# Kernel tuning notes

Hardware: AMD Instinct MI355X
Metric: run time of the kernel (lower is better)

Reference implementation:

```python
import jax, jax.numpy as jnp
import numpy as np

B, N, E, D, R, T, L = 4, 20000, 320000, 64, 64, 1000, 6
LN_EPS = 1e-5


def setup_inputs() -> dict:
    key = jax.random.key(0)
    ks = jax.random.split(key, 20)
    inp = {
        "edge_index": jax.random.randint(ks[0], (2, E), 0, N),
        "edge_type": jax.random.randint(ks[1], (E,), 0, R),
        "relation_representations": jax.random.normal(ks[2], (B, R, D), jnp.float32),
        "h_index": jax.random.randint(ks[3], (B,), 0, N),
        "r_index": jax.random.randint(ks[4], (B,), 0, R),
        "t_index": jax.random.randint(ks[5], (B, T), 0, N),
        "edge_weight": jnp.ones((E,), jnp.float32),
        # per-layer relation-projection MLP (Linear,ReLU,Linear)
        "rp_w1": jax.random.normal(ks[6], (L, D, D), jnp.float32) / np.sqrt(D),
        "rp_b1": jnp.zeros((L, D), jnp.float32),
        "rp_w2": jax.random.normal(ks[7], (L, D, D), jnp.float32) / np.sqrt(D),
        "rp_b2": jnp.zeros((L, D), jnp.float32),
        # per-layer update linear: concat([input, aggregated]) -> D
        "conv_w": jax.random.normal(ks[8], (L, 2 * D, D), jnp.float32) / np.sqrt(2 * D),
        "conv_b": jnp.zeros((L, D), jnp.float32),
        "ln_g": jnp.ones((L, D), jnp.float32),
        "ln_b": jnp.zeros((L, D), jnp.float32),
        # final MLP (num_mlp_layers=2): feature_dim = D (last hidden) + D (query) = 2D
        "mlp_w1": jax.random.normal(ks[9], (2 * D, 2 * D), jnp.float32) / np.sqrt(2 * D),
        "mlp_b1": jnp.zeros((2 * D,), jnp.float32),
        "mlp_w2": jax.random.normal(ks[10], (2 * D, 1), jnp.float32) / np.sqrt(2 * D),
        "mlp_b2": jnp.zeros((1,), jnp.float32),
    }
    return inp


def reference(edge_index, edge_type, relation_representations, h_index, r_index,
              t_index, edge_weight, rp_w1, rp_b1, rp_w2, rp_b2, conv_w, conv_b,
              ln_g, ln_b, mlp_w1, mlp_b1, mlp_w2, mlp_b2):
    # --- boundary: scatter query embedding onto source node per query ---
    query = relation_representations[jnp.arange(B), r_index]              # [B, D]
    boundary = jnp.zeros((B, N, D), jnp.float32).at[jnp.arange(B), h_index].add(query)
    src, dst = edge_index[0], edge_index[1]

    def layer(x, params):
        w1, b1, w2, b2, cw, cb, g, b = params
        # project_relations MLP on query relation representations
        rel = jax.nn.relu(jnp.einsum('brd,de->bre', relation_representations, w1) + b1)
        rel = jnp.einsum('brd,de->bre', rel, w2) + b2                     # [B, R, D]
        # distmult message: h[src] * rel[edge_type], weighted
        msg = x[:, src, :] * rel[:, edge_type, :] * edge_weight[None, :, None]  # [B, E, D]
        agg = jax.ops.segment_sum(msg.transpose(1, 0, 2), dst,
                                  num_segments=N).transpose(1, 0, 2)
        agg = agg + boundary                                              # boundary self-loop
        h = jnp.concatenate([x, agg], axis=-1) @ cw + cb                  # [B, N, D]
        mu = h.mean(-1, keepdims=True)
        var = h.var(-1, keepdims=True)
        h = (h - mu) * jax.lax.rsqrt(var + LN_EPS) * g + b                # layer norm
        h = jax.nn.relu(h)
        return h + x, None                                                # short_cut

    x, _ = jax.lax.scan(layer, boundary,
                        (rp_w1, rp_b1, rp_w2, rp_b2, conv_w, conv_b, ln_g, ln_b))
    node_query = jnp.broadcast_to(query[:, None, :], (B, N, D))
    output = jnp.concatenate([x, node_query], axis=-1)                    # [B, N, 2D]
    feat = jnp.take_along_axis(output, t_index[:, :, None], axis=1)       # [B, T, 2D]
    h = jax.nn.relu(feat @ mlp_w1 + mlp_b1)
    score = (h @ mlp_w2 + mlp_b2).squeeze(-1)                             # [B, T]
    return score
```

## Files before the change

### kernel.cpp

```cpp
#include <hip/hip_runtime.h>
#include <hip/hip_fp16.h>

#define NB 4
#define NN 20000
#define NE 320000
#define ND 64
#define NR 64
#define NT 1000
#define NL 6
#define LN_EPS 1e-5f
#define CAP 64

typedef _Float16 half8 __attribute__((ext_vector_type(8)));
typedef _Float16 half4v __attribute__((ext_vector_type(4)));
typedef float floatx4 __attribute__((ext_vector_type(4)));


__global__ void __launch_bounds__(256)
prep1(int* __restrict__ cnt,
      const float* __restrict__ cw, _Float16* __restrict__ cwt,
      const float* __restrict__ relrep, const int* __restrict__ r_index,
      float* __restrict__ query,
      const float* __restrict__ rp_w1, const float* __restrict__ rp_b1,
      const float* __restrict__ rp_w2, const float* __restrict__ rp_b2,
      __half* __restrict__ rel16) {
    int blk = blockIdx.x, tid = threadIdx.x;
    if (blk < 79) {
        int i = blk * 256 + tid;
        if (i < NN) cnt[i] = 0;
    } else if (blk < 271) {
        int i = (blk - 79) * 256 + tid;
        int l = i >> 13, rem = i & 8191, k = rem >> 6, n = rem & 63;
        cwt[l * 8192 + n * 128 + k] = (_Float16)cw[i];
    } else if (blk == 271) {
        int b = tid >> 6, d = tid & 63;
        query[tid] = relrep[(b * NR + r_index[b]) * ND + d];
    } else {
        int u = blk - 272;
        int l = u >> 6, r = u & 63;
        int b = tid >> 6, j = tid & 63;
        const float* w1 = rp_w1 + l * ND * ND;
        const float* w2 = rp_w2 + l * ND * ND;
        float xin = relrep[(b * NR + r) * ND + j];
        float acc = rp_b1[l * ND + j];
        #pragma unroll 8
        for (int k = 0; k < ND; ++k) acc += __shfl(xin, k) * w1[k * ND + j];
        float hmid = fmaxf(acc, 0.f);
        float outv = rp_b2[l * ND + j];
        #pragma unroll 8
        for (int k = 0; k < ND; ++k) outv += __shfl(hmid, k) * w2[k * ND + j];
        rel16[l * (NR * NB * ND) + (r * NB + b) * ND + j] = __float2half(outv);
    }
}

__global__ void __launch_bounds__(256)
prep2(const int* __restrict__ ei, const int* __restrict__ et,
      const float* __restrict__ ew, int* __restrict__ cnt,
      int4* __restrict__ epack) {
    int e = blockIdx.x * 256 + threadIdx.x;
    int d = ei[NE + e];
    int p = atomicAdd(&cnt[d], 1);
    if (p < CAP)
        epack[d * CAP + p] = make_int4(ei[e], et[e], __float_as_int(ew[e]), 0);
}

__device__ __forceinline__ float2 h2f(unsigned u) {
    __half2 h = *(__half2*)&u;
    return __half22float2(h);
}
__device__ __forceinline__ __half2 u2h2(unsigned u) { return *(__half2*)&u; }

__device__ __forceinline__ void conv_ln_epilogue(
        _Float16* A16, float* sD, int wv, int lane, int n,
        const _Float16* __restrict__ cwt, const float* __restrict__ cb,
        const float* __restrict__ g, const float* __restrict__ bb,
        __half* __restrict__ xo16) {
    __syncthreads();
    {
        int m = lane & 15, quad = lane >> 4;
        int ncol = wv * 16 + m;
        floatx4 acc = {0.f, 0.f, 0.f, 0.f};
        #pragma unroll
        for (int k0 = 0; k0 < 128; k0 += 32) {
            half8 a = *(const half8*)&A16[m * 136 + k0 + quad * 8];
            half8 bfr = *(const half8*)&cwt[ncol * 128 + k0 + quad * 8];
            acc = __builtin_amdgcn_mfma_f32_16x16x32_f16(a, bfr, acc, 0, 0, 0);
        }
        #pragma unroll
        for (int rg = 0; rg < 4; ++rg)
            sD[(quad * 4 + rg) * 65 + ncol] = acc[rg];
    }
    __syncthreads();
    float gl = g[lane], bl = bb[lane], cbl = cb[lane];
    #pragma unroll
    for (int b = 0; b < NB; ++b) {
        float acc = sD[(wv * 4 + b) * 65 + lane] + cbl;
        float s = acc, s2 = acc * acc;
        #pragma unroll
        for (int o = 32; o > 0; o >>= 1) { s += __shfl_xor(s, o); s2 += __shfl_xor(s2, o); }
        float mu  = s * (1.f / ND);
        float var = s2 * (1.f / ND) - mu * mu;
        float hn  = (acc - mu) * rsqrtf(var + LN_EPS) * gl + bl;
        float xvf = (float)A16[(wv * 4 + b) * 136 + lane];
        float v   = fmaxf(hn, 0.f) + xvf;
        xo16[(n * NB + b) * ND + lane] = __float2half(v);
    }
}

__global__ void __launch_bounds__(256)
fused_layer_first(const __half* __restrict__ rel16,
                  const int* __restrict__ cnt, const int4* __restrict__ epack,
                  const float* __restrict__ query, const int* __restrict__ h_index,
                  const _Float16* __restrict__ cwt, const float* __restrict__ cb,
                  const float* __restrict__ g, const float* __restrict__ bb,
                  __half* __restrict__ xo16) {
    __shared__ _Float16 A16[16 * 136];
    __shared__ float sD[16 * 65];
    int wv = threadIdx.x >> 6;
    int lane = threadIdx.x & 63;
    int n = blockIdx.x * 4 + wv;
    int cn = __builtin_amdgcn_readfirstlane(min(cnt[n], CAP));
    int bidx = lane >> 4, c4 = (lane & 15) << 2;
    int hb = h_index[bidx];

    const uint2* __restrict__ r2 = (const uint2*)rel16;
    float4 q4 = ((const float4*)query)[lane];
    half4v qh;
    qh.x = (_Float16)q4.x; qh.y = (_Float16)q4.y;
    qh.z = (_Float16)q4.z; qh.w = (_Float16)q4.w;
    float qx = (float)qh.x, qy = (float)qh.y, qz = (float)qh.z, qw = (float)qh.w;

    float4 agg4 = make_float4(0.f, 0.f, 0.f, 0.f);
    {
        int4 ed = make_int4(0, 0, 0, 0);
        if (lane < cn) ed = epack[n * CAP + lane];
        for (int j = 0; j < cn; ++j) {
            int s   = __builtin_amdgcn_readlane(ed.x, j);
            int t   = __builtin_amdgcn_readlane(ed.y, j);
            float w = __int_as_float(__builtin_amdgcn_readlane(ed.z, j));
            if (s == hb) {
                uint2 ra = r2[t * 64 + lane];
                float2 q0 = h2f(ra.x), q1 = h2f(ra.y);
                agg4.x = fmaf(qx * q0.x, w, agg4.x);
                agg4.y = fmaf(qy * q0.y, w, agg4.y);
                agg4.z = fmaf(qz * q1.x, w, agg4.z);
                agg4.w = fmaf(qw * q1.y, w, agg4.w);
            }
        }
    }
    if (n == hb) {
        agg4.x += q4.x; agg4.y += q4.y; agg4.z += q4.z; agg4.w += q4.w;
    }
    {
        int r = wv * 4 + bidx;
        half4v xh = {0, 0, 0, 0};
        if (n == hb) xh = qh;
        *(half4v*)&A16[r * 136 + c4] = xh;
        half4v ah;
        ah.x = (_Float16)agg4.x; ah.y = (_Float16)agg4.y;
        ah.z = (_Float16)agg4.z; ah.w = (_Float16)agg4.w;
        *(half4v*)&A16[r * 136 + 64 + c4] = ah;
    }
    conv_ln_epilogue(A16, sD, wv, lane, n, cwt, cb, g, bb, xo16);
}

__global__ void __launch_bounds__(256)
fused_layer(const __half* __restrict__ x16, const __half* __restrict__ rel16,
            const int* __restrict__ cnt, const int4* __restrict__ epack,
            const float* __restrict__ query, const int* __restrict__ h_index,
            const _Float16* __restrict__ cwt, const float* __restrict__ cb,
            const float* __restrict__ g, const float* __restrict__ bb,
            __half* __restrict__ xo16) {
    __shared__ _Float16 A16[16 * 136];
    __shared__ float sD[16 * 65];
    int wv = threadIdx.x >> 6;
    int lane = threadIdx.x & 63;
    int n = blockIdx.x * 4 + wv;
    int cn = __builtin_amdgcn_readfirstlane(min(cnt[n], CAP));
    int bidx = lane >> 4, c4 = (lane & 15) << 2;
    int hb = h_index[bidx];

    const uint2* __restrict__ x2 = (const uint2*)x16;
    const uint2* __restrict__ r2 = (const uint2*)rel16;

    uint2 xraw = x2[n * 64 + lane];

    float4 acc = make_float4(0.f, 0.f, 0.f, 0.f);
    {
        int4 ed = make_int4(0, 0, 0, 0);
        if (lane < cn) ed = epack[n * CAP + lane];
        for (int j = 0; j < cn; ++j) {
            int s   = __builtin_amdgcn_readlane(ed.x, j);
            int t   = __builtin_amdgcn_readlane(ed.y, j);
            float w = __int_as_float(__builtin_amdgcn_readlane(ed.z, j));
            uint2 xa = x2[s * 64 + lane];
            uint2 ra = r2[t * 64 + lane];
            __half2 p0 = __hmul2(u2h2(xa.x), u2h2(ra.x));
            __half2 p1 = __hmul2(u2h2(xa.y), u2h2(ra.y));
            acc.x = fmaf(__low2float(p0),  w, acc.x);
            acc.y = fmaf(__high2float(p0), w, acc.y);
            acc.z = fmaf(__low2float(p1),  w, acc.z);
            acc.w = fmaf(__high2float(p1), w, acc.w);
        }
    }
    if (n == hb) {
        const float4 q4 = ((const float4*)query)[lane];
        acc.x += q4.x; acc.y += q4.y; acc.z += q4.z; acc.w += q4.w;
    }
    {
        int r = wv * 4 + bidx;
        half4v ah;
        ah.x = (_Float16)acc.x; ah.y = (_Float16)acc.y;
        ah.z = (_Float16)acc.z; ah.w = (_Float16)acc.w;
        *(half4v*)&A16[r * 136 + 64 + c4] = ah;
        *(uint2*)&A16[r * 136 + c4] = xraw;
    }
    conv_ln_epilogue(A16, sD, wv, lane, n, cwt, cb, g, bb, xo16);
}

__global__ void final_score(const __half* __restrict__ x16, const float* __restrict__ query,
                            const int* __restrict__ t_index,
                            const float* __restrict__ w1, const float* __restrict__ b1,
                            const float* __restrict__ w2, const float* __restrict__ b2,
                            float* __restrict__ out) {
    int gid = blockIdx.x * 4 + (threadIdx.x >> 6);
    int lane = threadIdx.x & 63;
    int b = gid / NT;
    int ti = t_index[gid];
    float xv = __half2float(x16[(ti * NB + b) * ND + lane]);
    float qv = query[b * ND + lane];
    float a0 = b1[lane], a1 = b1[lane + 64];
    #pragma unroll 8
    for (int k = 0; k < ND; ++k) {
        float f = __shfl(xv, k);
        a0 += f * w1[k * 128 + lane];
        a1 += f * w1[k * 128 + lane + 64];
    }
    #pragma unroll 8
    for (int k = 0; k < ND; ++k) {
        float f = __shfl(qv, k);
        a0 += f * w1[(ND + k) * 128 + lane];
        a1 += f * w1[(ND + k) * 128 + lane + 64];
    }
    a0 = fmaxf(a0, 0.f);
    a1 = fmaxf(a1, 0.f);
    float p = a0 * w2[lane] + a1 * w2[lane + 64];
    #pragma unroll
    for (int o = 32; o > 0; o >>= 1) p += __shfl_xor(p, o);
    if (lane == 0) out[gid] = p + b2[0];
}

extern "C" void kernel_launch(void* const* d_in, const int* in_sizes, int n_in,
                              void* d_out, int out_size, void* d_ws, size_t ws_size,
                              hipStream_t stream) {
    const int*   edge_index  = (const int*)d_in[0];
    const int*   edge_type   = (const int*)d_in[1];
    const float* relrep      = (const float*)d_in[2];
    const int*   h_index     = (const int*)d_in[3];
    const int*   r_index     = (const int*)d_in[4];
    const int*   t_index     = (const int*)d_in[5];
    const float* edge_weight = (const float*)d_in[6];
    const float* rp_w1  = (const float*)d_in[7];
    const float* rp_b1  = (const float*)d_in[8];
    const float* rp_w2  = (const float*)d_in[9];
    const float* rp_b2  = (const float*)d_in[10];
    const float* conv_w = (const float*)d_in[11];
    const float* conv_b = (const float*)d_in[12];
    const float* ln_g   = (const float*)d_in[13];
    const float* ln_b   = (const float*)d_in[14];
    const float* mlp_w1 = (const float*)d_in[15];
    const float* mlp_b1 = (const float*)d_in[16];
    const float* mlp_w2 = (const float*)d_in[17];
    const float* mlp_b2 = (const float*)d_in[18];
    float* out = (float*)d_out;

    const int BND = NB * NN * ND;
    const int RELSZ = NR * NB * ND;
    float*    ws     = (float*)d_ws;
    float*    query  = ws;
    __half*   rel16  = (__half*)(query + 256);
    __half*   x16a   = rel16 + NL * RELSZ;
    __half*   x16b   = x16a + BND;
    _Float16* cwt16  = (_Float16*)(x16b + BND);
    int4*     epack  = (int4*)(cwt16 + NL * 8192);
    int*      cnt    = (int*)(epack + NN * CAP);

    prep1<<<656, 256, 0, stream>>>(cnt, conv_w, cwt16, relrep, r_index, query,
                                   rp_w1, rp_b1, rp_w2, rp_b2, rel16);
    prep2<<<NE / 256, 256, 0, stream>>>(edge_index, edge_type, edge_weight,
                                        cnt, epack);

    __half* mc = x16a; __half* mn = x16b;
    fused_layer_first<<<NN / 4, 256, 0, stream>>>(rel16, cnt, epack,
                                                  query, h_index,
                                                  cwt16, conv_b, ln_g, ln_b, mc);
    for (int l = 1; l < NL; ++l) {
        fused_layer<<<NN / 4, 256, 0, stream>>>(mc, rel16 + l * RELSZ, cnt, epack,
                                                query, h_index,
                                                cwt16 + l * 8192, conv_b + l * ND,
                                                ln_g + l * ND, ln_b + l * ND, mn);
        __half* th = mc; mc = mn; mn = th;
    }
    final_score<<<NB * NT / 4, 256, 0, stream>>>(mc, query, t_index,
                                                 mlp_w1, mlp_b1, mlp_w2, mlp_b2, out);
}
```

Before: 358.2 us.

## Stage per-layer relation table in LDS and double block size to eight nodes

Each block now cooperatively copies the layer's 32 KB fp16 relation table (R*B*D) into shared memory and serves per-edge relation gathers from LDS instead of global memory. Blocks grow from 4 to 8 waves (two groups of 4 nodes) to spread the staging cost over more nodes. This costs a 32 KB LDS copy per block and an extra barrier, which may cap occupancy and add traffic, though the table likely already sat in L2.

```diff
diff --git a/kernel.cpp b/kernel.cpp
--- a/kernel.cpp
+++ b/kernel.cpp
@@ -71,59 +71,71 @@
 __device__ __forceinline__ __half2 u2h2(unsigned u) { return *(__half2*)&u; }
 
 __device__ __forceinline__ void conv_ln_epilogue(
-        _Float16* A16, float* sD, int wv, int lane, int n,
+        _Float16* A16g, float* sDg, int wvl, int lane, int n,
         const _Float16* __restrict__ cwt, const float* __restrict__ cb,
         const float* __restrict__ g, const float* __restrict__ bb,
         __half* __restrict__ xo16) {
     __syncthreads();
     {
         int m = lane & 15, quad = lane >> 4;
-        int ncol = wv * 16 + m;
+        int ncol = wvl * 16 + m;
         floatx4 acc = {0.f, 0.f, 0.f, 0.f};
         #pragma unroll
         for (int k0 = 0; k0 < 128; k0 += 32) {
-            half8 a = *(const half8*)&A16[m * 136 + k0 + quad * 8];
+            half8 a = *(const half8*)&A16g[m * 136 + k0 + quad * 8];
             half8 bfr = *(const half8*)&cwt[ncol * 128 + k0 + quad * 8];
             acc = __builtin_amdgcn_mfma_f32_16x16x32_f16(a, bfr, acc, 0, 0, 0);
         }
         #pragma unroll
         for (int rg = 0; rg < 4; ++rg)
-            sD[(quad * 4 + rg) * 65 + ncol] = acc[rg];
+            sDg[(quad * 4 + rg) * 65 + ncol] = acc[rg];
     }
     __syncthreads();
     float gl = g[lane], bl = bb[lane], cbl = cb[lane];
     #pragma unroll
     for (int b = 0; b < NB; ++b) {
-        float acc = sD[(wv * 4 + b) * 65 + lane] + cbl;
+        float acc = sDg[(wvl * 4 + b) * 65 + lane] + cbl;
         float s = acc, s2 = acc * acc;
         #pragma unroll
         for (int o = 32; o > 0; o >>= 1) { s += __shfl_xor(s, o); s2 += __shfl_xor(s2, o); }
         float mu  = s * (1.f / ND);
         float var = s2 * (1.f / ND) - mu * mu;
         float hn  = (acc - mu) * rsqrtf(var + LN_EPS) * gl + bl;
-        float xvf = (float)A16[(wv * 4 + b) * 136 + lane];
+        float xvf = (float)A16g[(wvl * 4 + b) * 136 + lane];
         float v   = fmaxf(hn, 0.f) + xvf;
         xo16[(n * NB + b) * ND + lane] = __float2half(v);
     }
 }
 
-__global__ void __launch_bounds__(256)
+__global__ void __launch_bounds__(512)
 fused_layer_first(const __half* __restrict__ rel16,
                   const int* __restrict__ cnt, const int4* __restrict__ epack,
                   const float* __restrict__ query, const int* __restrict__ h_index,
                   const _Float16* __restrict__ cwt, const float* __restrict__ cb,
                   const float* __restrict__ g, const float* __restrict__ bb,
                   __half* __restrict__ xo16) {
-    __shared__ _Float16 A16[16 * 136];
-    __shared__ float sD[16 * 65];
-    int wv = threadIdx.x >> 6;
-    int lane = threadIdx.x & 63;
-    int n = blockIdx.x * 4 + wv;
+    __shared__ _Float16 relS[NR * NB * ND];
+    __shared__ _Float16 A16[2][16 * 136];
+    __shared__ float sD[2][16 * 65];
+    int tid = threadIdx.x;
+    int wv = tid >> 6, lane = tid & 63;
+    int grp = wv >> 2, wvl = wv & 3;
+    int n = blockIdx.x * 8 + wv;
     int cn = __builtin_amdgcn_readfirstlane(min(cnt[n], CAP));
     int bidx = lane >> 4, c4 = (lane & 15) << 2;
     int hb = h_index[bidx];
 
-    const uint2* __restrict__ r2 = (const uint2*)rel16;
+    int4 ed = make_int4(0, 0, 0, 0);
+    if (lane < cn) ed = epack[n * CAP + lane];
+
+    {
+        const uint4* rg4 = (const uint4*)rel16;
+        uint4* rs4 = (uint4*)relS;
+        #pragma unroll
+        for (int k = 0; k < 4; ++k) rs4[tid + 512 * k] = rg4[tid + 512 * k];
+    }
+    __syncthreads();
+
     float4 q4 = ((const float4*)query)[lane];
     half4v qh;
     qh.x = (_Float16)q4.x; qh.y = (_Float16)q4.y;
@@ -131,91 +143,96 @@
     float qx = (float)qh.x, qy = (float)qh.y, qz = (float)qh.z, qw = (float)qh.w;
 
     float4 agg4 = make_float4(0.f, 0.f, 0.f, 0.f);
-    {
-        int4 ed = make_int4(0, 0, 0, 0);
-        if (lane < cn) ed = epack[n * CAP + lane];
-        for (int j = 0; j < cn; ++j) {
-            int s   = __builtin_amdgcn_readlane(ed.x, j);
-            int t   = __builtin_amdgcn_readlane(ed.y, j);
-            float w = __int_as_float(__builtin_amdgcn_readlane(ed.z, j));
-            if (s == hb) {
-                uint2 ra = r2[t * 64 + lane];
-                float2 q0 = h2f(ra.x), q1 = h2f(ra.y);
-                agg4.x = fmaf(qx * q0.x, w, agg4.x);
-                agg4.y = fmaf(qy * q0.y, w, agg4.y);
-                agg4.z = fmaf(qz * q1.x, w, agg4.z);
-                agg4.w = fmaf(qw * q1.y, w, agg4.w);
-            }
+    const uint2* __restrict__ rS2 = (const uint2*)relS;
+    for (int j = 0; j < cn; ++j) {
+        int s   = __builtin_amdgcn_readlane(ed.x, j);
+        int t   = __builtin_amdgcn_readlane(ed.y, j);
+        float w = __int_as_float(__builtin_amdgcn_readlane(ed.z, j));
+        if (s == hb) {
+            uint2 ra = rS2[t * 64 + lane];
+            float2 q0 = h2f(ra.x), q1 = h2f(ra.y);
+            agg4.x = fmaf(qx * q0.x, w, agg4.x);
+            agg4.y = fmaf(qy * q0.y, w, agg4.y);
+            agg4.z = fmaf(qz * q1.x, w, agg4.z);
+            agg4.w = fmaf(qw * q1.y, w, agg4.w);
         }
     }
     if (n == hb) {
         agg4.x += q4.x; agg4.y += q4.y; agg4.z += q4.z; agg4.w += q4.w;
     }
     {
-        int r = wv * 4 + bidx;
+        int r = wvl * 4 + bidx;
         half4v xh = {0, 0, 0, 0};
         if (n == hb) xh = qh;
-        *(half4v*)&A16[r * 136 + c4] = xh;
+        *(half4v*)&A16[grp][r * 136 + c4] = xh;
         half4v ah;
         ah.x = (_Float16)agg4.x; ah.y = (_Float16)agg4.y;
         ah.z = (_Float16)agg4.z; ah.w = (_Float16)agg4.w;
-        *(half4v*)&A16[r * 136 + 64 + c4] = ah;
-    }
-    conv_ln_epilogue(A16, sD, wv, lane, n, cwt, cb, g, bb, xo16);
-}
-
-__global__ void __launch_bounds__(256)
+        *(half4v*)&A16[grp][r * 136 + 64 + c4] = ah;
+    }
+    conv_ln_epilogue(A16[grp], sD[grp], wvl, lane, n, cwt, cb, g, bb, xo16);
+}
+
+__global__ void __launch_bounds__(512)
 fused_layer(const __half* __restrict__ x16, const __half* __restrict__ rel16,
             const int* __restrict__ cnt, const int4* __restrict__ epack,
             const float* __restrict__ query, const int* __restrict__ h_index,
             const _Float16* __restrict__ cwt, const float* __restrict__ cb,
             const float* __restrict__ g, const float* __restrict__ bb,
             __half* __restrict__ xo16) {
-    __shared__ _Float16 A16[16 * 136];
-    __shared__ float sD[16 * 65];
-    int wv = threadIdx.x >> 6;
-    int lane = threadIdx.x & 63;
-    int n = blockIdx.x * 4 + wv;
+    __shared__ _Float16 relS[NR * NB * ND];
+    __shared__ _Float16 A16[2][16 * 136];
+    __shared__ float sD[2][16 * 65];
+    int tid = threadIdx.x;
+    int wv = tid >> 6, lane = tid & 63;
+    int grp = wv >> 2, wvl = wv & 3;
+    int n = blockIdx.x * 8 + wv;
     int cn = __builtin_amdgcn_readfirstlane(min(cnt[n], CAP));
     int bidx = lane >> 4, c4 = (lane & 15) << 2;
     int hb = h_index[bidx];
 
     const uint2* __restrict__ x2 = (const uint2*)x16;
-    const uint2* __restrict__ r2 = (const uint2*)rel16;
-
+
+    int4 ed = make_int4(0, 0, 0, 0);
+    if (lane < cn) ed = epack[n * CAP + lane];
     uint2 xraw = x2[n * 64 + lane];
 
+    {
+        const uint4* rg4 = (const uint4*)rel16;
+        uint4* rs4 = (uint4*)relS;
+        #pragma unroll
+        for (int k = 0; k < 4; ++k) rs4[tid + 512 * k] = rg4[tid + 512 * k];
+    }
+    __syncthreads();
+
     float4 acc = make_float4(0.f, 0.f, 0.f, 0.f);
-    {
-        int4 ed = make_int4(0, 0, 0, 0);
-        if (lane < cn) ed = epack[n * CAP + lane];
-        for (int j = 0; j < cn; ++j) {
-            int s   = __builtin_amdgcn_readlane(ed.x, j);
-            int t   = __builtin_amdgcn_readlane(ed.y, j);
-            float w = __int_as_float(__builtin_amdgcn_readlane(ed.z, j));
-            uint2 xa = x2[s * 64 + lane];
-            uint2 ra = r2[t * 64 + lane];
-            __half2 p0 = __hmul2(u2h2(xa.x), u2h2(ra.x));
-            __half2 p1 = __hmul2(u2h2(xa.y), u2h2(ra.y));
-            acc.x = fmaf(__low2float(p0),  w, acc.x);
-            acc.y = fmaf(__high2float(p0), w, acc.y);
-            acc.z = fmaf(__low2float(p1),  w, acc.z);
-            acc.w = fmaf(__high2float(p1), w, acc.w);
-        }
+    const uint2* __restrict__ rS2 = (const uint2*)relS;
+    for (int j = 0; j < cn; ++j) {
+        int s   = __builtin_amdgcn_readlane(ed.x, j);
+        int t   = __builtin_amdgcn_readlane(ed.y, j);
+        float w = __int_as_float(__builtin_amdgcn_readlane(ed.z, j));
+        uint2 xa = x2[s * 64 + lane];
+        uint2 ra = rS2[t * 64 + lane];
+        __half2 p0 = __hmul2(u2h2(xa.x), u2h2(ra.x));
+        __half2 p1 = __hmul2(u2h2(xa.y), u2h2(ra.y));
+        acc.x = fmaf(__low2float(p0),  w, acc.x);
+        acc.y = fmaf(__high2float(p0), w, acc.y);
+        acc.z = fmaf(__low2float(p1),  w, acc.z);
+        acc.w = fmaf(__high2float(p1), w, acc.w);
     }
     if (n == hb) {
         const float4 q4 = ((const float4*)query)[lane];
         acc.x += q4.x; acc.y += q4.y; acc.z += q4.z; acc.w += q4.w;
     }
     {
-        int r = wv * 4 + bidx;
+        int r = wvl * 4 + bidx;
         half4v ah;
         ah.x = (_Float16)acc.x; ah.y = (_Float16)acc.y;
         ah.z = (_Float16)acc.z; ah.w = (_Float16)acc.w;
-        *(half4v*)&A16[r * 136 + 64 + c4] = ah;
-        *(uint2*)&A16[r * 136 + c4] = xraw;
-    }
-    conv_ln_epilogue(A16, sD, wv, lane, n, cwt, cb, g, bb, xo16);
+        *(half4v*)&A16[grp][r * 136 + 64 + c4] = ah;
+        *(uint2*)&A16[grp][r * 136 + c4] = xraw;
+    }
+    conv_ln_epilogue(A16[grp], sD[grp], wvl, lane, n, cwt, cb, g, bb, xo16);
 }
 
 __global__ void final_score(const __half* __restrict__ x16, const float* __restrict__ query,
@@ -291,11 +308,11 @@
                                         cnt, epack);
 
     __half* mc = x16a; __half* mn = x16b;
-    fused_layer_first<<<NN / 4, 256, 0, stream>>>(rel16, cnt, epack,
+    fused_layer_first<<<NN / 8, 512, 0, stream>>>(rel16, cnt, epack,
                                                   query, h_index,
                                                   cwt16, conv_b, ln_g, ln_b, mc);
     for (int l = 1; l < NL; ++l) {
-        fused_layer<<<NN / 4, 256, 0, stream>>>(mc, rel16 + l * RELSZ, cnt, epack,
+        fused_layer<<<NN / 8, 512, 0, stream>>>(mc, rel16 + l * RELSZ, cnt, epack,
                                                 query, h_index,
                                                 cwt16 + l * 8192, conv_b + l * ND,
                                                 ln_g + l * ND, ln_b + l * ND, mn);
```

After: 429.1 us. 19.8% more time.

## Split edge gather across half-waves per batch and use 512-thread blocks

Applied to the files above, without the earlier changes.

The non-first layer kernel now loops over the four batches separately. In each step the two half-waves gather two different edges, using 4-byte loads of one batch slice, and their partial sums are combined with a cross-half shuffle. Blocks grow to 8 nodes (512 threads), with per-group shared-memory tiles for the MFMA/LayerNorm epilogue. The aim is more independent gathers in flight per wave. The cost is twice as many loop iterations and narrower, less vectorised loads, with padding reads when an odd edge count pairs with an empty lane.

```diff
diff --git a/kernel.cpp b/kernel.cpp
--- a/kernel.cpp
+++ b/kernel.cpp
@@ -71,37 +71,37 @@
 __device__ __forceinline__ __half2 u2h2(unsigned u) { return *(__half2*)&u; }
 
 __device__ __forceinline__ void conv_ln_epilogue(
-        _Float16* A16, float* sD, int wv, int lane, int n,
+        _Float16* A16g, float* sDg, int wvl, int lane, int n,
         const _Float16* __restrict__ cwt, const float* __restrict__ cb,
         const float* __restrict__ g, const float* __restrict__ bb,
         __half* __restrict__ xo16) {
     __syncthreads();
     {
         int m = lane & 15, quad = lane >> 4;
-        int ncol = wv * 16 + m;
+        int ncol = wvl * 16 + m;
         floatx4 acc = {0.f, 0.f, 0.f, 0.f};
         #pragma unroll
         for (int k0 = 0; k0 < 128; k0 += 32) {
-            half8 a = *(const half8*)&A16[m * 136 + k0 + quad * 8];
+            half8 a = *(const half8*)&A16g[m * 136 + k0 + quad * 8];
             half8 bfr = *(const half8*)&cwt[ncol * 128 + k0 + quad * 8];
             acc = __builtin_amdgcn_mfma_f32_16x16x32_f16(a, bfr, acc, 0, 0, 0);
         }
         #pragma unroll
         for (int rg = 0; rg < 4; ++rg)
-            sD[(quad * 4 + rg) * 65 + ncol] = acc[rg];
+            sDg[(quad * 4 + rg) * 65 + ncol] = acc[rg];
     }
     __syncthreads();
     float gl = g[lane], bl = bb[lane], cbl = cb[lane];
     #pragma unroll
     for (int b = 0; b < NB; ++b) {
-        float acc = sD[(wv * 4 + b) * 65 + lane] + cbl;
+        float acc = sDg[(wvl * 4 + b) * 65 + lane] + cbl;
         float s = acc, s2 = acc * acc;
         #pragma unroll
         for (int o = 32; o > 0; o >>= 1) { s += __shfl_xor(s, o); s2 += __shfl_xor(s2, o); }
         float mu  = s * (1.f / ND);
         float var = s2 * (1.f / ND) - mu * mu;
         float hn  = (acc - mu) * rsqrtf(var + LN_EPS) * gl + bl;
-        float xvf = (float)A16[(wv * 4 + b) * 136 + lane];
+        float xvf = (float)A16g[(wvl * 4 + b) * 136 + lane];
         float v   = fmaxf(hn, 0.f) + xvf;
         xo16[(n * NB + b) * ND + lane] = __float2half(v);
     }
@@ -164,58 +164,62 @@
     conv_ln_epilogue(A16, sD, wv, lane, n, cwt, cb, g, bb, xo16);
 }
 
-__global__ void __launch_bounds__(256)
+__global__ void __launch_bounds__(512)
 fused_layer(const __half* __restrict__ x16, const __half* __restrict__ rel16,
             const int* __restrict__ cnt, const int4* __restrict__ epack,
             const float* __restrict__ query, const int* __restrict__ h_index,
             const _Float16* __restrict__ cwt, const float* __restrict__ cb,
             const float* __restrict__ g, const float* __restrict__ bb,
             __half* __restrict__ xo16) {
-    __shared__ _Float16 A16[16 * 136];
-    __shared__ float sD[16 * 65];
-    int wv = threadIdx.x >> 6;
-    int lane = threadIdx.x & 63;
-    int n = blockIdx.x * 4 + wv;
+    __shared__ _Float16 A16[2][16 * 136];
+    __shared__ float sD[2][16 * 65];
+    int tid = threadIdx.x;
+    int wv = tid >> 6, lane = tid & 63;
+    int grp = wv >> 2, wvl = wv & 3;
+    int n = blockIdx.x * 8 + wv;
     int cn = __builtin_amdgcn_readfirstlane(min(cnt[n], CAP));
-    int bidx = lane >> 4, c4 = (lane & 15) << 2;
-    int hb = h_index[bidx];
-
-    const uint2* __restrict__ x2 = (const uint2*)x16;
-    const uint2* __restrict__ r2 = (const uint2*)rel16;
-
-    uint2 xraw = x2[n * 64 + lane];
-
-    float4 acc = make_float4(0.f, 0.f, 0.f, 0.f);
-    {
-        int4 ed = make_int4(0, 0, 0, 0);
-        if (lane < cn) ed = epack[n * CAP + lane];
-        for (int j = 0; j < cn; ++j) {
-            int s   = __builtin_amdgcn_readlane(ed.x, j);
-            int t   = __builtin_amdgcn_readlane(ed.y, j);
-            float w = __int_as_float(__builtin_amdgcn_readlane(ed.z, j));
-            uint2 xa = x2[s * 64 + lane];
-            uint2 ra = r2[t * 64 + lane];
-            __half2 p0 = __hmul2(u2h2(xa.x), u2h2(ra.x));
-            __half2 p1 = __hmul2(u2h2(xa.y), u2h2(ra.y));
-            acc.x = fmaf(__low2float(p0),  w, acc.x);
-            acc.y = fmaf(__high2float(p0), w, acc.y);
-            acc.z = fmaf(__low2float(p1),  w, acc.z);
-            acc.w = fmaf(__high2float(p1), w, acc.w);
-        }
-    }
-    if (n == hb) {
-        const float4 q4 = ((const float4*)query)[lane];
-        acc.x += q4.x; acc.y += q4.y; acc.z += q4.z; acc.w += q4.w;
-    }
-    {
-        int r = wv * 4 + bidx;
-        half4v ah;
-        ah.x = (_Float16)acc.x; ah.y = (_Float16)acc.y;
-        ah.z = (_Float16)acc.z; ah.w = (_Float16)acc.w;
-        *(half4v*)&A16[r * 136 + 64 + c4] = ah;
-        *(uint2*)&A16[r * 136 + c4] = xraw;
-    }
-    conv_ln_epilogue(A16, sD, wv, lane, n, cwt, cb, g, bb, xo16);
+    int hf = lane >> 5, sub = lane & 31;
+
+    const uint* __restrict__ xu = (const uint*)x16;
+    const uint* __restrict__ ru = (const uint*)rel16;
+
+    int4 ed = make_int4(0, 0, 0, 0);
+    if (lane < cn) ed = epack[n * CAP + lane];
+
+    for (int b = 0; b < NB; ++b) {
+        float ax = 0.f, ay = 0.f;
+        for (int j = 0; j < cn; j += 2) {
+            int s0 = __builtin_amdgcn_readlane(ed.x, j);
+            int s1 = __builtin_amdgcn_readlane(ed.x, j + 1);
+            int t0 = __builtin_amdgcn_readlane(ed.y, j);
+            int t1 = __builtin_amdgcn_readlane(ed.y, j + 1);
+            int w0 = __builtin_amdgcn_readlane(ed.z, j);
+            int w1 = __builtin_amdgcn_readlane(ed.z, j + 1);
+            int s = hf ? s1 : s0;
+            int t = hf ? t1 : t0;
+            float w = __int_as_float(hf ? w1 : w0);
+            uint xa = xu[(s * NB + b) * 32 + sub];
+            uint ra = ru[(t * NB + b) * 32 + sub];
+            __half2 p = __hmul2(u2h2(xa), u2h2(ra));
+            ax = fmaf(__low2float(p),  w, ax);
+            ay = fmaf(__high2float(p), w, ay);
+        }
+        ax += __shfl_xor(ax, 32);
+        ay += __shfl_xor(ay, 32);
+        if (n == h_index[b]) {
+            float2 q = ((const float2*)query)[b * 32 + sub];
+            ax += q.x; ay += q.y;
+        }
+        int r = wvl * 4 + b;
+        if (hf == 0) {
+            __half2 ah;
+            ah.x = __float2half(ax); ah.y = __float2half(ay);
+            *(__half2*)&A16[grp][r * 136 + 64 + 2 * sub] = ah;
+            uint xr = xu[(n * NB + b) * 32 + sub];
+            *(uint*)&A16[grp][r * 136 + 2 * sub] = xr;
+        }
+    }
+    conv_ln_epilogue(A16[grp], sD[grp], wvl, lane, n, cwt, cb, g, bb, xo16);
 }
 
 __global__ void final_score(const __half* __restrict__ x16, const float* __restrict__ query,
@@ -295,7 +299,7 @@
                                                   query, h_index,
                                                   cwt16, conv_b, ln_g, ln_b, mc);
     for (int l = 1; l < NL; ++l) {
-        fused_layer<<<NN / 4, 256, 0, stream>>>(mc, rel16 + l * RELSZ, cnt, epack,
+        fused_layer<<<NN / 8, 512, 0, stream>>>(mc, rel16 + l * RELSZ, cnt, epack,
                                                 query, h_index,
                                                 cwt16 + l * 8192, conv_b + l * ND,
                                                 ln_g + l * ND, ln_b + l * ND, mn);
```

New measurement: 520.6 us. 45.3% more time.

## Switch node features to batch-major layout and split fused layer per batch

Applied to the files above, without the earlier changes.

Changes the x and relation buffers from node-major [N,B,D] to batch-major [B,N,D] and packs source and edge type into one int, shrinking edge records from int4 to int2. The fused layer now runs one batch per block over 16 nodes, with half-waves gathering 128-byte rows per edge, and pairs adjacent blocks of the same batch. The aim is to cut edge-metadata traffic and improve L2 locality, since each block now touches only one batch's 2.5MB feature slab. The cost is that edge lists are re-read once per batch, and only half the waves do the MFMA step.

```diff
diff --git a/kernel.cpp b/kernel.cpp
--- a/kernel.cpp
+++ b/kernel.cpp
@@ -49,19 +49,20 @@
         float outv = rp_b2[l * ND + j];
         #pragma unroll 8
         for (int k = 0; k < ND; ++k) outv += __shfl(hmid, k) * w2[k * ND + j];
-        rel16[l * (NR * NB * ND) + (r * NB + b) * ND + j] = __float2half(outv);
+        rel16[l * (NR * NB * ND) + (b * NR + r) * ND + j] = __float2half(outv);
     }
 }
 
 __global__ void __launch_bounds__(256)
 prep2(const int* __restrict__ ei, const int* __restrict__ et,
       const float* __restrict__ ew, int* __restrict__ cnt,
-      int4* __restrict__ epack) {
+      int2* __restrict__ ep2) {
     int e = blockIdx.x * 256 + threadIdx.x;
     int d = ei[NE + e];
     int p = atomicAdd(&cnt[d], 1);
     if (p < CAP)
-        epack[d * CAP + p] = make_int4(ei[e], et[e], __float_as_int(ew[e]), 0);
+        ep2[d * CAP + p] = make_int2(ei[e] | (et[e] << 16),
+                                     __float_as_int(ew[e]));
 }
 
 __device__ __forceinline__ float2 h2f(unsigned u) {
@@ -70,7 +71,7 @@
 }
 __device__ __forceinline__ __half2 u2h2(unsigned u) { return *(__half2*)&u; }
 
-__device__ __forceinline__ void conv_ln_epilogue(
+__device__ __forceinline__ void conv_ln_epilogue4(
         _Float16* A16, float* sD, int wv, int lane, int n,
         const _Float16* __restrict__ cwt, const float* __restrict__ cb,
         const float* __restrict__ g, const float* __restrict__ bb,
@@ -103,13 +104,13 @@
         float hn  = (acc - mu) * rsqrtf(var + LN_EPS) * gl + bl;
         float xvf = (float)A16[(wv * 4 + b) * 136 + lane];
         float v   = fmaxf(hn, 0.f) + xvf;
-        xo16[(n * NB + b) * ND + lane] = __float2half(v);
+        xo16[(b * NN + n) * ND + lane] = __float2half(v);
     }
 }
 
 __global__ void __launch_bounds__(256)
 fused_layer_first(const __half* __restrict__ rel16,
-                  const int* __restrict__ cnt, const int4* __restrict__ epack,
+                  const int* __restrict__ cnt, const int2* __restrict__ ep2,
                   const float* __restrict__ query, const int* __restrict__ h_index,
                   const _Float16* __restrict__ cwt, const float* __restrict__ cb,
                   const float* __restrict__ g, const float* __restrict__ bb,
@@ -132,14 +133,14 @@
 
     float4 agg4 = make_float4(0.f, 0.f, 0.f, 0.f);
     {
-        int4 ed = make_int4(0, 0, 0, 0);
-        if (lane < cn) ed = epack[n * CAP + lane];
+        int2 ed = make_int2(0, 0);
+        if (lane < cn) ed = ep2[n * CAP + lane];
         for (int j = 0; j < cn; ++j) {
-            int s   = __builtin_amdgcn_readlane(ed.x, j);
-            int t   = __builtin_amdgcn_readlane(ed.y, j);
-            float w = __int_as_float(__builtin_amdgcn_readlane(ed.z, j));
+            int p   = __builtin_amdgcn_readlane(ed.x, j);
+            float w = __int_as_float(__builtin_amdgcn_readlane(ed.y, j));
+            int s = p & 0xffff, t = p >> 16;
             if (s == hb) {
-                uint2 ra = r2[t * 64 + lane];
+                uint2 ra = r2[(bidx * NR + t) * 16 + (lane & 15)];
                 float2 q0 = h2f(ra.x), q1 = h2f(ra.y);
                 agg4.x = fmaf(qx * q0.x, w, agg4.x);
                 agg4.y = fmaf(qy * q0.y, w, agg4.y);
@@ -161,61 +162,98 @@
         ah.z = (_Float16)agg4.z; ah.w = (_Float16)agg4.w;
         *(half4v*)&A16[r * 136 + 64 + c4] = ah;
     }
-    conv_ln_epilogue(A16, sD, wv, lane, n, cwt, cb, g, bb, xo16);
-}
-
-__global__ void __launch_bounds__(256)
+    conv_ln_epilogue4(A16, sD, wv, lane, n, cwt, cb, g, bb, xo16);
+}
+
+__global__ void __launch_bounds__(512)
 fused_layer(const __half* __restrict__ x16, const __half* __restrict__ rel16,
-            const int* __restrict__ cnt, const int4* __restrict__ epack,
+            const int* __restrict__ cnt, const int2* __restrict__ ep2,
             const float* __restrict__ query, const int* __restrict__ h_index,
             const _Float16* __restrict__ cwt, const float* __restrict__ cb,
             const float* __restrict__ g, const float* __restrict__ bb,
             __half* __restrict__ xo16) {
     __shared__ _Float16 A16[16 * 136];
     __shared__ float sD[16 * 65];
-    int wv = threadIdx.x >> 6;
-    int lane = threadIdx.x & 63;
-    int n = blockIdx.x * 4 + wv;
-    int cn = __builtin_amdgcn_readfirstlane(min(cnt[n], CAP));
-    int bidx = lane >> 4, c4 = (lane & 15) << 2;
-    int hb = h_index[bidx];
-
-    const uint2* __restrict__ x2 = (const uint2*)x16;
-    const uint2* __restrict__ r2 = (const uint2*)rel16;
-
-    uint2 xraw = x2[n * 64 + lane];
-
-    float4 acc = make_float4(0.f, 0.f, 0.f, 0.f);
+    int tid = threadIdx.x;
+    int wv = tid >> 6, lane = tid & 63;
+    int hf = lane >> 5, sub = lane & 31;
+    int blk = blockIdx.x;
+    int b = (blk & 7) >> 1;
+    int i = ((blk >> 3) << 1) + (blk & 1);
+    int node_base = i * 16;
+    int r = wv * 2 + hf;
+    int n = node_base + r;
+    int cnH = min(cnt[n], CAP);
+    int cmax = max(cnH, __shfl_xor(cnH, 32));
+    int hb = h_index[b];
+
+    const uint* __restrict__ xu = (const uint*)x16;
+    const uint* __restrict__ ru = (const uint*)rel16;
+
+    float ax = 0.f, ay = 0.f;
+    for (int c0 = 0; c0 < cmax; c0 += 32) {
+        int2 ed = make_int2(0, 0);
+        int idx = c0 + sub;
+        if (idx < cnH) ed = ep2[n * CAP + idx];
+        int jend = min(cmax - c0, 32);
+        for (int j = 0; j < jend; ++j) {
+            int pA = __builtin_amdgcn_readlane(ed.x, j);
+            int pB = __builtin_amdgcn_readlane(ed.x, j + 32);
+            int wA = __builtin_amdgcn_readlane(ed.y, j);
+            int wB = __builtin_amdgcn_readlane(ed.y, j + 32);
+            int p   = hf ? pB : pA;
+            float w = __int_as_float(hf ? wB : wA);
+            int s = p & 0xffff, t = p >> 16;
+            uint xa = xu[(b * NN + s) * 32 + sub];
+            uint ra = ru[(b * NR + t) * 32 + sub];
+            __half2 pr = __hmul2(u2h2(xa), u2h2(ra));
+            ax = fmaf(__low2float(pr),  w, ax);
+            ay = fmaf(__high2float(pr), w, ay);
+        }
+    }
+    if (n == hb) {
+        float2 q = ((const float2*)query)[b * 32 + sub];
+        ax += q.x; ay += q.y;
+    }
     {
-        int4 ed = make_int4(0, 0, 0, 0);
-        if (lane < cn) ed = epack[n * CAP + lane];
-        for (int j = 0; j < cn; ++j) {
-            int s   = __builtin_amdgcn_readlane(ed.x, j);
-            int t   = __builtin_amdgcn_readlane(ed.y, j);
-            float w = __int_as_float(__builtin_amdgcn_readlane(ed.z, j));
-            uint2 xa = x2[s * 64 + lane];
-            uint2 ra = r2[t * 64 + lane];
-            __half2 p0 = __hmul2(u2h2(xa.x), u2h2(ra.x));
-            __half2 p1 = __hmul2(u2h2(xa.y), u2h2(ra.y));
-            acc.x = fmaf(__low2float(p0),  w, acc.x);
-            acc.y = fmaf(__high2float(p0), w, acc.y);
-            acc.z = fmaf(__low2float(p1),  w, acc.z);
-            acc.w = fmaf(__high2float(p1), w, acc.w);
+        __half2 ah;
+        ah.x = __float2half(ax); ah.y = __float2half(ay);
+        *(__half2*)&A16[r * 136 + 64 + 2 * sub] = ah;
+        uint xr = xu[(b * NN + n) * 32 + sub];
+        *(uint*)&A16[r * 136 + 2 * sub] = xr;
+    }
+    __syncthreads();
+    if (wv < 4) {
+        int m = lane & 15, quad = lane >> 4;
+        int ncol = wv * 16 + m;
+        floatx4 acc4 = {0.f, 0.f, 0.f, 0.f};
+        #pragma unroll
+        for (int k0 = 0; k0 < 128; k0 += 32) {
+            half8 a = *(const half8*)&A16[m * 136 + k0 + quad * 8];
+            half8 bfr = *(const half8*)&cwt[ncol * 128 + k0 + quad * 8];
+            acc4 = __builtin_amdgcn_mfma_f32_16x16x32_f16(a, bfr, acc4, 0, 0, 0);
         }
-    }
-    if (n == hb) {
-        const float4 q4 = ((const float4*)query)[lane];
-        acc.x += q4.x; acc.y += q4.y; acc.z += q4.z; acc.w += q4.w;
-    }
-    {
-        int r = wv * 4 + bidx;
-        half4v ah;
-        ah.x = (_Float16)acc.x; ah.y = (_Float16)acc.y;
-        ah.z = (_Float16)acc.z; ah.w = (_Float16)acc.w;
-        *(half4v*)&A16[r * 136 + 64 + c4] = ah;
-        *(uint2*)&A16[r * 136 + c4] = xraw;
-    }
-    conv_ln_epilogue(A16, sD, wv, lane, n, cwt, cb, g, bb, xo16);
+        #pragma unroll
+        for (int rg = 0; rg < 4; ++rg)
+            sD[(quad * 4 + rg) * 65 + ncol] = acc4[rg];
+    }
+    __syncthreads();
+    float gl = g[lane], bl = bb[lane], cbl = cb[lane];
+    #pragma unroll
+    for (int r2i = 0; r2i < 2; ++r2i) {
+        int row = wv * 2 + r2i;
+        int nn = node_base + row;
+        float acc = sD[row * 65 + lane] + cbl;
+        float s = acc, s2 = acc * acc;
+        #pragma unroll
+        for (int o = 32; o > 0; o >>= 1) { s += __shfl_xor(s, o); s2 += __shfl_xor(s2, o); }
+        float mu  = s * (1.f / ND);
+        float var = s2 * (1.f / ND) - mu * mu;
+        float hn  = (acc - mu) * rsqrtf(var + LN_EPS) * gl + bl;
+        float xvf = (float)A16[row * 136 + lane];
+        float v   = fmaxf(hn, 0.f) + xvf;
+        xo16[(b * NN + nn) * ND + lane] = __float2half(v);
+    }
 }
 
 __global__ void final_score(const __half* __restrict__ x16, const float* __restrict__ query,
@@ -227,7 +265,7 @@
     int lane = threadIdx.x & 63;
     int b = gid / NT;
     int ti = t_index[gid];
-    float xv = __half2float(x16[(ti * NB + b) * ND + lane]);
+    float xv = __half2float(x16[(b * NN + ti) * ND + lane]);
     float qv = query[b * ND + lane];
     float a0 = b1[lane], a1 = b1[lane + 64];
     #pragma unroll 8
@@ -282,7 +320,7 @@
     __half*   x16a   = rel16 + NL * RELSZ;
     __half*   x16b   = x16a + BND;
     _Float16* cwt16  = (_Float16*)(x16b + BND);
-    int4*     epack  = (int4*)(cwt16 + NL * 8192);
+    int2*     epack  = (int2*)(cwt16 + NL * 8192);
     int*      cnt    = (int*)(epack + NN * CAP);
 
     prep1<<<656, 256, 0, stream>>>(cnt, conv_w, cwt16, relrep, r_index, query,
@@ -295,10 +333,10 @@
                                                   query, h_index,
                                                   cwt16, conv_b, ln_g, ln_b, mc);
     for (int l = 1; l < NL; ++l) {
-        fused_layer<<<NN / 4, 256, 0, stream>>>(mc, rel16 + l * RELSZ, cnt, epack,
-                                                query, h_index,
-                                                cwt16 + l * 8192, conv_b + l * ND,
-                                                ln_g + l * ND, ln_b + l * ND, mn);
+        fused_layer<<<NN / 16 * NB, 512, 0, stream>>>(mc, rel16 + l * RELSZ, cnt, epack,
+                                                      query, h_index,
+                                                      cwt16 + l * 8192, conv_b + l * ND,
+                                                      ln_g + l * ND, ln_b + l * ND, mn);
         __half* th = mc; mc = mn; mn = th;
     }
     final_score<<<NB * NT / 4, 256, 0, stream>>>(mc, query, t_index,
```

New measurement: 441.5 us. +23.3%, slower.
